# Kernel optimization log

Measured on AMD Instinct MI355X. Metric: run time of the kernel, lower is better.

Reference implementation:

```python
import math
import jax, jax.numpy as jnp
import numpy as np

B, S, D_MODEL = 4, 1024, 512
D_BAR, C_ONSET, N_HEADS = 256, 32, 8
T_ONSET, POOL = 8192, 8


def setup_inputs() -> dict:
    key = jax.random.key(0)
    ks = jax.random.split(key, 16)
    p = lambda i, shape: jax.random.normal(ks[i], shape, dtype=jnp.float32) * 0.05
    return {
        "token_embs": jax.random.normal(ks[0], (B, S, D_MODEL), dtype=jnp.float32),
        "onset_1d": jax.random.uniform(ks[1], (B, T_ONSET, C_ONSET), dtype=jnp.float32),
        "bar_mask": jax.random.bernoulli(ks[2], 0.0625, (B, S)),  # ~1 bar / 16 tokens
        "Wih_note": p(3, (3 * D_BAR, D_MODEL)),
        "Whh_note": p(4, (3 * D_BAR, D_BAR)),
        "bih_note": p(5, (3 * D_BAR,)),
        "bhh_note": p(6, (3 * D_BAR,)),
        "Wih_bar": p(7, (3 * D_BAR, D_BAR)),
        "Whh_bar": p(8, (3 * D_BAR, D_BAR)),
        "bih_bar": p(9, (3 * D_BAR,)),
        "bhh_bar": p(10, (3 * D_BAR,)),
        "Wq": p(11, (D_BAR, D_BAR)),
        "bq": p(12, (D_BAR,)),
        "Wk": p(13, (D_BAR, C_ONSET)),
        "bk": p(14, (D_BAR,)),
        "pos_bias_scale": jnp.float32(2.5),
    }


def _gru_cell(x, h, Wih, Whh, bih, bhh):
    # torch nn.GRU cell, gate order (r, z, n)
    gi = x @ Wih.T + bih
    gh = h @ Whh.T + bhh
    ir, iz, inn = jnp.split(gi, 3, axis=-1)
    hr, hz, hn = jnp.split(gh, 3, axis=-1)
    r = jax.nn.sigmoid(ir + hr)
    z = jax.nn.sigmoid(iz + hz)
    n = jnp.tanh(inn + r * hn)
    return (1.0 - z) * n + z * h


def _sinusoidal_pe(T, C, dtype):
    half = C // 2
    pos = jnp.arange(T, dtype=dtype)
    div = jnp.exp(jnp.arange(half, dtype=dtype) * (-math.log(10000.0) / half))
    ang = pos[:, None] * div[None, :]  # [T, half]
    # interleave sin/cos -> [T, C] (C even)
    return jnp.stack([jnp.sin(ang), jnp.cos(ang)], axis=-1).reshape(T, C)


def _forward(token_embs, onset_1d, bar_mask, Wih_note, Whh_note, bih_note, bhh_note,
             Wih_bar, Whh_bar, bih_bar, bhh_bar, Wq, bq, Wk, bk, pos_bias_scale):
    Bc, Sc, _ = token_embs.shape
    d_bar = Whh_bar.shape[1]
    H = N_HEADS
    dh = d_bar // H
    dtype = token_embs.dtype

    # --- audio keys: avg_pool1d(k=8,s=8) + sinusoidal PE + projection ---
    T = onset_1d.shape[1]
    pooled = onset_1d.reshape(Bc, T // POOL, POOL, onset_1d.shape[2]).mean(axis=2)  # [B,T_oct,C]
    T_oct = pooled.shape[1]
    pe = _sinusoidal_pe(T_oct, pooled.shape[2], dtype)
    K = (pooled + pe[None]) @ Wk.T + bk  # [B,T_oct,d_bar]

    # --- fused note-GRU / bar-GRU scan over sequence positions ---
    # Segment semantics: bar tokens are excluded from note-GRU segments; at a
    # <bar> position the note hidden (= bar summary; zero for empty segments)
    # feeds one bar-GRU step, then the note hidden resets to zero.
    def step(carry, xs):
        h_note, g_bar = carry
        x, m = xs  # x: [B,D], m: [B] bool
        h_next = _gru_cell(x, h_note, Wih_note, Whh_note, bih_note, bhh_note)
        g_next = _gru_cell(h_note, g_bar, Wih_bar, Whh_bar, bih_bar, bhh_bar)
        m_ = m[:, None]
        g_out = jnp.where(m_, g_next, g_bar)
        h_out = jnp.where(m_, jnp.zeros_like(h_next), h_next)
        return (h_out, g_out), g_out

    zeros = jnp.zeros((Bc, d_bar), dtype=dtype)
    (_, g_end), g_seq = jax.lax.scan(
        step, (zeros, zeros),
        (token_embs.transpose(1, 0, 2), bar_mask.T))
    h_bar_carried = g_seq.transpose(1, 0, 2)  # [B,S,d_bar]: h_bar after most recent bar <= s
    h_bar_final = g_end[None]                 # [1,B,d_bar]

    # --- cross-attention com_t (computed densely, masked to <bar> positions) ---
    Q = (h_bar_carried @ Wq.T + bq).reshape(Bc, Sc, H, dh)
    K4 = K.reshape(Bc, T_oct, H, dh)
    scores = jnp.einsum('bshd,bthd->bsht', Q, K4) / math.sqrt(dh)
    time_pos = jnp.linspace(0.0, 1.0, T_oct, dtype=dtype)
    scores = scores - pos_bias_scale * time_pos  # broadcast pos bias over t
    attn = jax.nn.softmax(scores, axis=-1)
    com = jnp.sum(attn.mean(axis=2) * time_pos, axis=-1)  # [B,S]
    com_t_all = jnp.where(bar_mask, com, 0.0)[..., None]  # [B,S,1]

    return com_t_all, h_bar_final, h_bar_carried


def reference(token_embs, onset_1d, bar_mask, Wih_note, Whh_note, bih_note, bhh_note,
              Wih_bar, Whh_bar, bih_bar, bhh_bar, Wq, bq, Wk, bk, pos_bias_scale):
    return _forward(token_embs, onset_1d, bar_mask, Wih_note, Whh_note, bih_note, bhh_note,
                    Wih_bar, Whh_bar, bih_bar, bhh_bar, Wq, bq, Wk, bk, pos_bias_scale)
```

## Files before the change

### kernel.cpp

```cpp
#include <hip/hip_runtime.h>
#include <hip/hip_bf16.h>
#include <math.h>

#define NB 4
#define SEQ 1024
#define DM 512
#define DB 256
#define G3 768
#define CO 32
#define TONS 8192
#define POOLN 8
#define TOCT 1024
#define NH 8
#define DHD 32

#define RKT 5
#define LKT 3

#define OFF_GI     0u
#define OFF_GIBAR  3145728u
#define OFF_HEND   6291456u
#define OFF_GALL   7340032u
#define OFF_KMAT   8388608u
#define OFF_WFN    9437184u
#define OFF_WFB    9535488u
#define OFF_WFIHN  9633792u
#define OFF_WFIHB  9830400u
#define OFF_INT_BYTES 39714816u

#define OUT_FINAL 4096
#define OUT_CARR  5120

typedef __attribute__((ext_vector_type(8))) short short8v;
typedef __attribute__((ext_vector_type(4))) float f32x4;

__device__ __forceinline__ unsigned int bf16rne(float f) {
    unsigned int u = __float_as_uint(f);
    return (u + 0x7fffu + ((u >> 16) & 1u)) >> 16;
}
__device__ __forceinline__ float fsigm(float x) {
    return __fdividef(1.f, 1.f + __expf(-x));
}
__device__ __forceinline__ float ftanh(float x) {
    return 1.f - __fdividef(2.f, __expf(2.f * x) + 1.f);
}

__device__ void wfrag_job(const float* __restrict__ W, uint4* __restrict__ out,
                          int Kdim, int KTN, int idx) {
    if (idx >= 48 * KTN * 64) return;
    int lane = idx & 63;
    int TK = idx >> 6;
    int T = TK / KTN, Kt = TK % KTN;
    int row = 16 * T + (lane & 15);
    int kb = 32 * Kt + (lane >> 4) * 8;
    const float* wr = W + (size_t)row * Kdim + kb;
    uint4 u;
    u.x = bf16rne(wr[0]) | (bf16rne(wr[1]) << 16);
    u.y = bf16rne(wr[2]) | (bf16rne(wr[3]) << 16);
    u.z = bf16rne(wr[4]) | (bf16rne(wr[5]) << 16);
    u.w = bf16rne(wr[6]) | (bf16rne(wr[7]) << 16);
    out[idx] = u;
}

__global__ __launch_bounds__(256) void k_prep(const unsigned char* __restrict__ mraw,
        int* __restrict__ pos, int* __restrict__ lastk, int* __restrict__ nmask,
        int* __restrict__ sS, int* __restrict__ sLen, int* __restrict__ sC,
        int* __restrict__ nseg,
        const float* __restrict__ Whh_n, uint4* __restrict__ wfn,
        const float* __restrict__ Whh_b, uint4* __restrict__ wfb,
        const float* __restrict__ Wih_n, uint4* __restrict__ wfihn,
        const float* __restrict__ Wih_b, uint4* __restrict__ wfihb,
        const float* __restrict__ onset, const float* __restrict__ Wk,
        const float* __restrict__ bk, float* __restrict__ Kmat) {
    int bid = blockIdx.x;
    int tid = threadIdx.x;
    if (bid == 0) {
        __shared__ int rnz[8];
        __shared__ int gt1;
        __shared__ int mode;
        __shared__ int snm[NB];
        if (tid < 8) rnz[tid] = 0;
        if (tid == 0) gt1 = 0;
        __syncthreads();
        for (int i = tid; i < NB * SEQ; i += 256) {
            unsigned char v = mraw[i];
            if (v) {
                rnz[i & 7] = 1;
                if (v > 1) gt1 = 1;
            }
        }
        __syncthreads();
        if (tid == 0) {
            bool lowhalf = rnz[0] | rnz[1] | rnz[4] | rnz[5];
            bool hihalf  = rnz[2] | rnz[3] | rnz[6] | rnz[7];
            int m;
            if (hihalf && !lowhalf) {
                m = (rnz[2] | rnz[3]) ? 3 : 4;
            } else if (gt1) {
                m = 5;
            } else if (rnz[1] | rnz[3] | rnz[5] | rnz[7]) {
                m = 0;
            } else if (rnz[4]) {
                m = 1;
            } else if (rnz[0]) {
                m = 2;
            } else {
                m = 0;
            }
            mode = m;
        }
        __syncthreads();
        if (tid < NB) {
            int b = tid;
            int cnt = 0;
            for (int t = 0; t < SEQ; ++t) {
                int idx = b * SEQ + t;
                int mv;
                switch (mode) {
                    case 0:  mv = mraw[idx] != 0; break;
                    case 1:  mv = ((const int*)mraw)[idx] != 0; break;
                    case 2:  mv = ((const long long*)mraw)[idx] != 0LL; break;
                    case 3:  mv = ((const float*)mraw)[idx] != 0.f; break;
                    case 4:  mv = ((const double*)mraw)[idx] != 0.0; break;
                    default: mv = ((const unsigned short*)mraw)[idx] != 0; break;
                }
                if (mv) { pos[b * SEQ + cnt] = t; ++cnt; }
                lastk[idx] = cnt - 1;
            }
            nmask[b] = cnt;
            snm[b] = cnt;
        }
        __syncthreads();
        if (tid < NB) {
            int b = tid;
            int base = 0;
            for (int x = 0; x < b; ++x) base += snm[x];
            int cnt = snm[b];
            for (int k = 0; k < cnt; ++k) {
                int e = pos[b * SEQ + k];
                int s = (k == 0) ? 0 : (pos[b * SEQ + k - 1] + 1);
                sS[base + k]   = b * SEQ + s;
                sLen[base + k] = e - s;
                sC[base + k]   = b * SEQ + k;
            }
        }
        __syncthreads();
        if (tid == 0) {
            int t = 0;
            for (int x = 0; x < NB; ++x) t += snm[x];
            *nseg = t;
        }
    } else if (bid <= 96) {
        wfrag_job(Whh_n, wfn, DB, 8, (bid - 1) * 256 + tid);
    } else if (bid <= 192) {
        wfrag_job(Whh_b, wfb, DB, 8, (bid - 97) * 256 + tid);
    } else if (bid <= 384) {
        wfrag_job(Wih_n, wfihn, DM, 16, (bid - 193) * 256 + tid);
    } else if (bid <= 480) {
        wfrag_job(Wih_b, wfihb, DB, 8, (bid - 385) * 256 + tid);
    } else {
        __shared__ float xin[4][CO];
        int sub = tid >> 6;
        int t64 = tid & 63;
        int bt = (bid - 481) * 4 + sub;
        int b = bt >> 10, t = bt & 1023;
        if (t64 < CO) {
            float s = 0.f;
            const float* base = onset + ((size_t)b * TONS + (size_t)t * POOLN) * CO + t64;
#pragma unroll
            for (int p = 0; p < POOLN; ++p) s += base[p * CO];
            s *= (1.f / POOLN);
            int j = t64 >> 1;
            float dv = __expf(-logf(10000.f) * (float)j / 16.f);
            float ang = (float)t * dv;
            s += (t64 & 1) ? __cosf(ang) : __sinf(ang);
            xin[sub][t64] = s;
        }
        __syncthreads();
        for (int n = t64; n < DB; n += 64) {
            float acc = bk[n];
            const float* wr = Wk + (size_t)n * CO;
#pragma unroll
            for (int c = 0; c < CO; ++c) acc += xin[sub][c] * wr[c];
            Kmat[(size_t)bt * DB + n] = acc;
        }
    }
}

template<bool LIM>
__global__ __launch_bounds__(256) void k_gemm_mfma(int Kdim, int KTN,
        const float* __restrict__ A, const uint4* __restrict__ Bf,
        const float* __restrict__ bias, float* __restrict__ C,
        const int* __restrict__ nmask) {
    int bm = blockIdx.x * 64, bn = blockIdx.y * 64;
    if (LIM) {
        int b = bm >> 10;
        if ((bm & 1023) >= nmask[b]) return;
    }
    int tid = threadIdx.x;
    int w = tid >> 6;
    int lane = tid & 63;
    int arow = bm + 16 * w + (lane & 15);
    int kofs = (lane >> 4) * 8;
    f32x4 acc[4];
#pragma unroll
    for (int nt = 0; nt < 4; ++nt) acc[nt] = (f32x4){0.f, 0.f, 0.f, 0.f};
    for (int kc = 0; kc < KTN; ++kc) {
        const float* ap = A + (size_t)arow * Kdim + kc * 32 + kofs;
        float4 p0 = *reinterpret_cast<const float4*>(ap);
        float4 p1 = *reinterpret_cast<const float4*>(ap + 4);
        uint4 au;
        au.x = bf16rne(p0.x) | (bf16rne(p0.y) << 16);
        au.y = bf16rne(p0.z) | (bf16rne(p0.w) << 16);
        au.z = bf16rne(p1.x) | (bf16rne(p1.y) << 16);
        au.w = bf16rne(p1.z) | (bf16rne(p1.w) << 16);
        short8v a = __builtin_bit_cast(short8v, au);
#pragma unroll
        for (int nt = 0; nt < 4; ++nt) {
            int T = (bn >> 4) + nt;
            uint4 u = Bf[(size_t)(T * KTN + kc) * 64 + lane];
            short8v bv = __builtin_bit_cast(short8v, u);
            acc[nt] = __builtin_amdgcn_mfma_f32_16x16x32_bf16(a, bv, acc[nt], 0, 0, 0);
        }
    }
    int crow = bm + 16 * w + (lane >> 4) * 4;
#pragma unroll
    for (int nt = 0; nt < 4; ++nt) {
        int col = bn + 16 * nt + (lane & 15);
        float bv = bias[col];
#pragma unroll
        for (int r = 0; r < 4; ++r)
            C[(size_t)(crow + r) * G3 + col] = acc[nt][r] + bv;
    }
}

template<int MODE>
__global__ __launch_bounds__(512, 1) void k_gru(
        const uint4* __restrict__ wf, const float* __restrict__ bhh,
        const float* __restrict__ gx_src,
        const int* __restrict__ sS, const int* __restrict__ sLen,
        const int* __restrict__ sC, const int* __restrict__ nseg_p,
        const int* __restrict__ nmask, float* __restrict__ outp) {
    int bg = blockIdx.x;
    int nseg = (MODE == 0) ? *nseg_p : NB;
    if (16 * bg >= nseg) return;
    int tid = threadIdx.x;
    int w = tid >> 6;
    int lane = tid & 63;
    int lhi = lane >> 4, c = lane & 15;

    __shared__ __align__(16) unsigned short hfrag[8 * 64 * 8];
    __shared__ __align__(16) uint4 wlds[8 * 6 * LKT * 64];

    uint4 wreg[6][RKT];
#pragma unroll
    for (int t = 0; t < 6; ++t) {
        int T = 16 * (t >> 1) + 2 * w + (t & 1);
#pragma unroll
        for (int kt = 0; kt < RKT; ++kt)
            wreg[t][kt] = wf[(size_t)(T * 8 + kt) * 64 + lane];
#pragma unroll
        for (int kt = 0; kt < LKT; ++kt)
            wlds[((w * 6 + t) * LKT + kt) * 64 + lane] = wf[(size_t)(T * 8 + RKT + kt) * 64 + lane];
    }

    int ss_r[4], len_r[4], sc_r[4];
#pragma unroll
    for (int r = 0; r < 4; ++r) {
        int m = 4 * lhi + r;
        int gs = 16 * bg + m;
        if (MODE == 0) {
            bool v = gs < nseg;
            ss_r[r]  = v ? sS[gs] : 0;
            len_r[r] = v ? sLen[gs] : 0;
            sc_r[r]  = v ? sC[gs] : 0;
        } else {
            bool v = m < NB;
            ss_r[r]  = v ? m * SEQ : 0;
            len_r[r] = v ? nmask[m] : 0;
            sc_r[r]  = 0;
        }
    }
    int mx = 0;
    for (int q = 0; q < 16; ++q) {
        int gs = 16 * bg + q;
        int L = (MODE == 0) ? ((gs < nseg) ? sLen[gs] : 0)
                            : ((q < NB) ? nmask[q] : 0);
        mx = max(mx, L);
    }
    float bh[3][2];
#pragma unroll
    for (int g = 0; g < 3; ++g)
#pragma unroll
        for (int ii = 0; ii < 2; ++ii)
            bh[g][ii] = bhh[g * 256 + 32 * w + 16 * ii + c];
    float h[4][2] = {};

#define LOADGX(dst, step)                                                        \
    {                                                                            \
        int i_ = (step);                                                         \
        _Pragma("unroll")                                                        \
        for (int r = 0; r < 4; ++r) {                                            \
            int row = (i_ < len_r[r]) ? (ss_r[r] + i_) : ss_r[r];                \
            const float* gp = gx_src + (size_t)row * G3 + 32 * w + c;            \
            _Pragma("unroll")                                                    \
            for (int g = 0; g < 3; ++g)                                          \
                _Pragma("unroll")                                                \
                for (int ii = 0; ii < 2; ++ii)                                   \
                    dst[g][ii][r] = gp[g * 256 + 16 * ii];                       \
        }                                                                        \
    }

#define GRU_STEP(I, GX)                                                          \
    {                                                                            \
        int i_ = (I);                                                            \
        f32x4 acc[6];                                                            \
        _Pragma("unroll")                                                        \
        for (int t = 0; t < 6; ++t) acc[t] = (f32x4){0.f, 0.f, 0.f, 0.f};        \
        if (i_ > 0) {                                                            \
            const short8v* hf8 = (const short8v*)hfrag;                          \
            _Pragma("unroll")                                                    \
            for (int kt = 0; kt < 8; ++kt) {                                     \
                short8v a = hf8[kt * 64 + lane];                                 \
                if (kt < RKT) {                                                  \
                    _Pragma("unroll")                                            \
                    for (int t = 0; t < 6; ++t) {                                \
                        short8v bv = __builtin_bit_cast(short8v, wreg[t][kt]);   \
                        acc[t] = __builtin_amdgcn_mfma_f32_16x16x32_bf16(        \
                                a, bv, acc[t], 0, 0, 0);                         \
                    }                                                            \
                } else {                                                         \
                    _Pragma("unroll")                                            \
                    for (int t = 0; t < 6; ++t) {                                \
                        uint4 u = wlds[((w * 6 + t) * LKT + (kt - RKT)) * 64 + lane]; \
                        short8v bv = __builtin_bit_cast(short8v, u);             \
                        acc[t] = __builtin_amdgcn_mfma_f32_16x16x32_bf16(        \
                                a, bv, acc[t], 0, 0, 0);                         \
                    }                                                            \
                }                                                                \
            }                                                                    \
        }                                                                        \
        _Pragma("unroll")                                                        \
        for (int r = 0; r < 4; ++r) {                                            \
            _Pragma("unroll")                                                    \
            for (int ii = 0; ii < 2; ++ii) {                                     \
                float rr = fsigm(GX[0][ii][r] + bh[0][ii] + acc[0 + ii][r]);     \
                float zz = fsigm(GX[1][ii][r] + bh[1][ii] + acc[2 + ii][r]);     \
                float nn = ftanh(GX[2][ii][r] + rr * (bh[2][ii] + acc[4 + ii][r])); \
                float hv = (1.f - zz) * nn + zz * h[r][ii];                      \
                bool act = i_ < len_r[r];                                        \
                hv = act ? hv : h[r][ii];                                        \
                h[r][ii] = hv;                                                   \
                if (MODE == 1) {                                                 \
                    if (lhi == 0 && act) {                                       \
                        int j = 32 * w + 16 * ii + c;                            \
                        outp[(size_t)(ss_r[r] + i_) * DB + j] = hv;              \
                    }                                                            \
                }                                                                \
            }                                                                    \
        }                                                                        \
        __syncthreads();                                                         \
        _Pragma("unroll")                                                        \
        for (int r = 0; r < 4; ++r)                                              \
            _Pragma("unroll")                                                    \
            for (int ii = 0; ii < 2; ++ii) {                                     \
                int j = 32 * w + 16 * ii + c;                                    \
                int m = 4 * lhi + r;                                             \
                int lp = m + 16 * ((j >> 3) & 3);                                \
                hfrag[(size_t)(w * 64 + lp) * 8 + (j & 7)] =                     \
                    (unsigned short)bf16rne(h[r][ii]);                           \
            }                                                                    \
        __syncthreads();                                                         \
    }

    float gxa[3][2][4], gxb[3][2][4];
    LOADGX(gxa, 0)
    for (int i = 0; i < mx; i += 2) {
        LOADGX(gxb, i + 1)
        GRU_STEP(i, gxa)
        LOADGX(gxa, i + 2)
        GRU_STEP(i + 1, gxb)
    }
#undef LOADGX
#undef GRU_STEP
    if (MODE == 0) {
#pragma unroll
        for (int r = 0; r < 4; ++r) {
            int gs = 16 * bg + 4 * lhi + r;
            if (gs < nseg) {
#pragma unroll
                for (int ii = 0; ii < 2; ++ii)
                    outp[(size_t)sc_r[r] * DB + 32 * w + 16 * ii + c] = h[r][ii];
            }
        }
    }
}

__global__ __launch_bounds__(256) void k_fillattn(const float* __restrict__ gall,
        const int* __restrict__ lastk, const int* __restrict__ nmask,
        const int* __restrict__ pos,
        const float* __restrict__ Wq, const float* __restrict__ bq,
        const float* __restrict__ Kmat, const float* __restrict__ pbs_ptr,
        float* __restrict__ out) {
    int bt = blockIdx.x;
    int b = bt >> 10, t = bt & 1023;
    int tid = threadIdx.x;
    int lk = lastk[bt];
    float v = (lk >= 0) ? gall[((size_t)b * SEQ + lk) * DB + tid] : 0.f;
    out[OUT_CARR + (size_t)bt * DB + tid] = v;
    if (tid == 0) out[bt] = 0.f;
    if (t == 0) {
        int nm = nmask[b];
        float fv = (nm > 0) ? gall[((size_t)b * SEQ + nm - 1) * DB + tid] : 0.f;
        out[OUT_FINAL + b * DB + tid] = fv;
    }
    bool is_mask = (lk >= 0) && (pos[b * SEQ + lk] == t);
    if (!is_mask) return;
    int k = lk;
    __shared__ float q[DB];
    __shared__ float grow[DB];
    __shared__ float sc[NH][TOCT];
    __shared__ float comh[NH];
    grow[tid] = gall[((size_t)b * SEQ + k) * DB + tid];
    __syncthreads();
    {
        float acc = bq[tid];
        const float* wr = Wq + (size_t)tid * DB;
#pragma unroll 4
        for (int j = 0; j < DB; ++j) acc += grow[j] * wr[j];
        q[tid] = acc;
    }
    __syncthreads();
    float pbs = *pbs_ptr;
    const float scale = 0.17677669529663687f;
    for (int tt = tid; tt < TOCT; tt += 256) {
        const float* kr = Kmat + ((size_t)b * TOCT + tt) * DB;
        float tp = (float)tt * (1.f / 1023.f);
#pragma unroll
        for (int h = 0; h < NH; ++h) {
            float acc = 0.f;
#pragma unroll
            for (int d = 0; d < DHD; ++d) acc += q[h * DHD + d] * kr[h * DHD + d];
            sc[h][tt] = acc * scale - pbs * tp;
        }
    }
    __syncthreads();
    int hh = tid >> 5, l = tid & 31;
    float mx = -1e30f;
    for (int tt = l; tt < TOCT; tt += 32) mx = fmaxf(mx, sc[hh][tt]);
#pragma unroll
    for (int o = 16; o > 0; o >>= 1) mx = fmaxf(mx, __shfl_xor(mx, o, 32));
    float se = 0.f, sw = 0.f;
    for (int tt = l; tt < TOCT; tt += 32) {
        float e = __expf(sc[hh][tt] - mx);
        se += e;
        sw += e * ((float)tt * (1.f / 1023.f));
    }
#pragma unroll
    for (int o = 16; o > 0; o >>= 1) { se += __shfl_xor(se, o, 32); sw += __shfl_xor(sw, o, 32); }
    if (l == 0) comh[hh] = sw / se;
    __syncthreads();
    if (tid == 0) {
        float cm = 0.f;
#pragma unroll
        for (int h = 0; h < NH; ++h) cm += comh[h];
        out[b * SEQ + t] = cm * (1.f / NH);
    }
}

extern "C" void kernel_launch(void* const* d_in, const int* in_sizes, int n_in,
                              void* d_out, int out_size, void* d_ws, size_t ws_size,
                              hipStream_t stream) {
    const float* te    = (const float*)d_in[0];
    const float* onset = (const float*)d_in[1];
    const unsigned char* mask = (const unsigned char*)d_in[2];
    const float* Wih_n = (const float*)d_in[3];
    const float* Whh_n = (const float*)d_in[4];
    const float* bih_n = (const float*)d_in[5];
    const float* bhh_n = (const float*)d_in[6];
    const float* Wih_b = (const float*)d_in[7];
    const float* Whh_b = (const float*)d_in[8];
    const float* bih_b = (const float*)d_in[9];
    const float* bhh_b = (const float*)d_in[10];
    const float* Wq    = (const float*)d_in[11];
    const float* bq    = (const float*)d_in[12];
    const float* Wk    = (const float*)d_in[13];
    const float* bk    = (const float*)d_in[14];
    const float* pbs   = (const float*)d_in[15];
    float* out = (float*)d_out;

    float* ws    = (float*)d_ws;
    float* gi    = ws + OFF_GI;
    float* gibar = ws + OFF_GIBAR;
    float* hend  = ws + OFF_HEND;
    float* gall  = ws + OFF_GALL;
    float* kmat  = ws + OFF_KMAT;
    uint4* wfn   = (uint4*)(ws + OFF_WFN);
    uint4* wfb   = (uint4*)(ws + OFF_WFB);
    uint4* wfihn = (uint4*)(ws + OFF_WFIHN);
    uint4* wfihb = (uint4*)(ws + OFF_WFIHB);
    int* ipos    = (int*)((char*)d_ws + OFF_INT_BYTES);
    int* ilastk  = ipos + NB * SEQ;
    int* inmask  = ilastk + NB * SEQ;
    int* isS     = inmask + NB;
    int* isLen   = isS + NB * SEQ;
    int* isC     = isLen + NB * SEQ;
    int* inseg   = isC + NB * SEQ;

    k_prep<<<1505, 256, 0, stream>>>(mask, ipos, ilastk, inmask, isS, isLen, isC, inseg,
                                     Whh_n, wfn, Whh_b, wfb, Wih_n, wfihn, Wih_b, wfihb,
                                     onset, Wk, bk, kmat);
    k_gemm_mfma<false><<<dim3(64, 12), 256, 0, stream>>>(DM, 16, te, wfihn, bih_n, gi, inmask);
    k_gru<0><<<256, 512, 0, stream>>>(wfn, bhh_n, gi, isS, isLen, isC, inseg, inmask, hend);
    k_gemm_mfma<true><<<dim3(64, 12), 256, 0, stream>>>(DB, 8, hend, wfihb, bih_b, gibar, inmask);
    k_gru<1><<<1, 512, 0, stream>>>(wfb, bhh_b, gibar, isS, isLen, isC, inseg, inmask, gall);
    k_fillattn<<<NB * SEQ, 256, 0, stream>>>(gall, ilastk, inmask, ipos, Wq, bq, kmat, pbs, out);
}
```

Measured before the change: 964.8 us.

## Fuse note GRU, bar input projection and bar GRU with flag-based streaming

Merges the note-level GRU, the bar input-projection GEMM and the bar-level GRU into a single persistent launch. Block 0 runs the bar GRU and polls per-segment ready flags, while the other blocks run note segments, compute the bar gate inputs in-register with MFMA, and publish them with release stores. This lets the serial bar recurrence overlap with note-GRU work and removes two launches and the intermediate h_end buffer. The cost is inter-block spin-waiting, which depends on all blocks being co-resident and risks a deadlock or a guarded timeout. Block 0 is also the bar GRU, and it contends for the device with 256 note blocks.

```diff
diff --git a/kernel.cpp b/kernel.cpp
--- a/kernel.cpp
+++ b/kernel.cpp
@@ -65,7 +65,7 @@
 __global__ __launch_bounds__(256) void k_prep(const unsigned char* __restrict__ mraw,
         int* __restrict__ pos, int* __restrict__ lastk, int* __restrict__ nmask,
         int* __restrict__ sS, int* __restrict__ sLen, int* __restrict__ sC,
-        int* __restrict__ nseg,
+        int* __restrict__ nseg, int* __restrict__ ibase, int* __restrict__ iflag,
         const float* __restrict__ Whh_n, uint4* __restrict__ wfn,
         const float* __restrict__ Whh_b, uint4* __restrict__ wfb,
         const float* __restrict__ Wih_n, uint4* __restrict__ wfihn,
@@ -75,6 +75,7 @@
     int bid = blockIdx.x;
     int tid = threadIdx.x;
     if (bid == 0) {
+        for (int i = tid; i < NB * SEQ; i += 256) iflag[i] = 0;
         __shared__ int rnz[8];
         __shared__ int gt1;
         __shared__ int mode;
@@ -135,6 +136,7 @@
             int b = tid;
             int base = 0;
             for (int x = 0; x < b; ++x) base += snm[x];
+            ibase[b] = base;
             int cnt = snm[b];
             for (int k = 0; k < cnt; ++k) {
                 int e = pos[b * SEQ + k];
@@ -187,16 +189,10 @@
     }
 }
 
-template<bool LIM>
 __global__ __launch_bounds__(256) void k_gemm_mfma(int Kdim, int KTN,
         const float* __restrict__ A, const uint4* __restrict__ Bf,
-        const float* __restrict__ bias, float* __restrict__ C,
-        const int* __restrict__ nmask) {
+        const float* __restrict__ bias, float* __restrict__ C) {
     int bm = blockIdx.x * 64, bn = blockIdx.y * 64;
-    if (LIM) {
-        int b = bm >> 10;
-        if ((bm & 1023) >= nmask[b]) return;
-    }
     int tid = threadIdx.x;
     int w = tid >> 6;
     int lane = tid & 63;
@@ -234,16 +230,17 @@
     }
 }
 
-template<int MODE>
-__global__ __launch_bounds__(512, 1) void k_gru(
-        const uint4* __restrict__ wf, const float* __restrict__ bhh,
-        const float* __restrict__ gx_src,
+__global__ __launch_bounds__(512, 1) void k_gru_fused(
+        const uint4* __restrict__ wfn, const float* __restrict__ bhh_n,
+        const float* __restrict__ gi,
+        const uint4* __restrict__ wfb, const float* __restrict__ bhh_b,
+        float* __restrict__ gibar,
+        const uint4* __restrict__ wfihb, const float* __restrict__ bih_b,
         const int* __restrict__ sS, const int* __restrict__ sLen,
         const int* __restrict__ sC, const int* __restrict__ nseg_p,
-        const int* __restrict__ nmask, float* __restrict__ outp) {
-    int bg = blockIdx.x;
-    int nseg = (MODE == 0) ? *nseg_p : NB;
-    if (16 * bg >= nseg) return;
+        const int* __restrict__ nmask, const int* __restrict__ ibase,
+        int* __restrict__ iflag, float* __restrict__ gall) {
+    int bid = blockIdx.x;
     int tid = threadIdx.x;
     int w = tid >> 6;
     int lane = tid & 63;
@@ -252,6 +249,15 @@
     __shared__ __align__(16) unsigned short hfrag[8 * 64 * 8];
     __shared__ __align__(16) uint4 wlds[8 * 6 * LKT * 64];
 
+    const int MODE = (bid == 0) ? 1 : 0;
+    int bg = bid - 1;
+    int nseg = *nseg_p;
+    if (MODE == 0 && 16 * bg >= nseg) return;
+
+    const uint4* wf = (MODE == 0) ? wfn : wfb;
+    const float* bhh = (MODE == 0) ? bhh_n : bhh_b;
+    const float* gx_src = (MODE == 0) ? gi : gibar;
+
     uint4 wreg[6][RKT];
 #pragma unroll
     for (int t = 0; t < 6; ++t) {
@@ -268,8 +274,8 @@
 #pragma unroll
     for (int r = 0; r < 4; ++r) {
         int m = 4 * lhi + r;
-        int gs = 16 * bg + m;
         if (MODE == 0) {
+            int gs = 16 * bg + m;
             bool v = gs < nseg;
             ss_r[r]  = v ? sS[gs] : 0;
             len_r[r] = v ? sLen[gs] : 0;
@@ -283,9 +289,13 @@
     }
     int mx = 0;
     for (int q = 0; q < 16; ++q) {
-        int gs = 16 * bg + q;
-        int L = (MODE == 0) ? ((gs < nseg) ? sLen[gs] : 0)
-                            : ((q < NB) ? nmask[q] : 0);
+        int L;
+        if (MODE == 0) {
+            int gs = 16 * bg + q;
+            L = (gs < nseg) ? sLen[gs] : 0;
+        } else {
+            L = (q < NB) ? nmask[q] : 0;
+        }
         mx = max(mx, L);
     }
     float bh[3][2];
@@ -295,6 +305,24 @@
         for (int ii = 0; ii < 2; ++ii)
             bh[g][ii] = bhh[g * 256 + 32 * w + 16 * ii + c];
     float h[4][2] = {};
+
+#define POLLSTEP(X)                                                              \
+    if (MODE == 1) {                                                             \
+        if (tid < NB) {                                                          \
+            int nm = nmask[tid];                                                 \
+            if (nm > 0) {                                                        \
+                int x_ = (X); if (x_ > nm - 1) x_ = nm - 1;                      \
+                int idx = ibase[tid] + x_;                                       \
+                long long guard = 0;                                             \
+                while (__hip_atomic_load(&iflag[idx], __ATOMIC_ACQUIRE,          \
+                                         __HIP_MEMORY_SCOPE_AGENT) == 0) {       \
+                    if (++guard > 200000000LL) break;                            \
+                    __builtin_amdgcn_s_sleep(2);                                 \
+                }                                                                \
+            }                                                                    \
+        }                                                                        \
+        __syncthreads();                                                         \
+    }
 
 #define LOADGX(dst, step)                                                        \
     {                                                                            \
@@ -354,7 +382,7 @@
                 if (MODE == 1) {                                                 \
                     if (lhi == 0 && act) {                                       \
                         int j = 32 * w + 16 * ii + c;                            \
-                        outp[(size_t)(ss_r[r] + i_) * DB + j] = hv;              \
+                        gall[(size_t)(ss_r[r] + i_) * DB + j] = hv;              \
                     }                                                            \
                 }                                                                \
             }                                                                    \
@@ -374,24 +402,55 @@
     }
 
     float gxa[3][2][4], gxb[3][2][4];
+    POLLSTEP(0)
     LOADGX(gxa, 0)
     for (int i = 0; i < mx; i += 2) {
+        POLLSTEP(i + 1)
         LOADGX(gxb, i + 1)
         GRU_STEP(i, gxa)
+        POLLSTEP(i + 2)
         LOADGX(gxa, i + 2)
         GRU_STEP(i + 1, gxb)
     }
+#undef POLLSTEP
 #undef LOADGX
 #undef GRU_STEP
+
     if (MODE == 0) {
-#pragma unroll
-        for (int r = 0; r < 4; ++r) {
-            int gs = 16 * bg + 4 * lhi + r;
-            if (gs < nseg) {
-#pragma unroll
-                for (int ii = 0; ii < 2; ++ii)
-                    outp[(size_t)sc_r[r] * DB + 32 * w + 16 * ii + c] = h[r][ii];
+        f32x4 acc[6];
+#pragma unroll
+        for (int t = 0; t < 6; ++t) acc[t] = (f32x4){0.f, 0.f, 0.f, 0.f};
+        const short8v* hf8 = (const short8v*)hfrag;
+#pragma unroll
+        for (int kt = 0; kt < 8; ++kt) {
+            short8v a = hf8[kt * 64 + lane];
+#pragma unroll
+            for (int t = 0; t < 6; ++t) {
+                int T = 16 * (t >> 1) + 2 * w + (t & 1);
+                uint4 u = wfihb[(size_t)(T * 8 + kt) * 64 + lane];
+                short8v bv = __builtin_bit_cast(short8v, u);
+                acc[t] = __builtin_amdgcn_mfma_f32_16x16x32_bf16(a, bv, acc[t], 0, 0, 0);
             }
+        }
+#pragma unroll
+        for (int t = 0; t < 6; ++t) {
+            int T = 16 * (t >> 1) + 2 * w + (t & 1);
+            int col = 16 * T + c;
+            float bv = bih_b[col];
+#pragma unroll
+            for (int r = 0; r < 4; ++r) {
+                int gs = 16 * bg + 4 * lhi + r;
+                if (gs < nseg)
+                    gibar[(size_t)sc_r[r] * G3 + col] = acc[t][r] + bv;
+            }
+        }
+        __syncthreads();
+        __threadfence();
+        if (tid < 16) {
+            int gs = 16 * bg + tid;
+            if (gs < nseg)
+                __hip_atomic_store(&iflag[gs], 1, __ATOMIC_RELEASE,
+                                   __HIP_MEMORY_SCOPE_AGENT);
         }
     }
 }
@@ -492,7 +551,6 @@
     float* ws    = (float*)d_ws;
     float* gi    = ws + OFF_GI;
     float* gibar = ws + OFF_GIBAR;
-    float* hend  = ws + OFF_HEND;
     float* gall  = ws + OFF_GALL;
     float* kmat  = ws + OFF_KMAT;
     uint4* wfn   = (uint4*)(ws + OFF_WFN);
@@ -506,13 +564,17 @@
     int* isLen   = isS + NB * SEQ;
     int* isC     = isLen + NB * SEQ;
     int* inseg   = isC + NB * SEQ;
+    int* ibase   = inseg + 1;
+    int* iflag   = ibase + 8;
 
     k_prep<<<1505, 256, 0, stream>>>(mask, ipos, ilastk, inmask, isS, isLen, isC, inseg,
+                                     ibase, iflag,
                                      Whh_n, wfn, Whh_b, wfb, Wih_n, wfihn, Wih_b, wfihb,
                                      onset, Wk, bk, kmat);
-    k_gemm_mfma<false><<<dim3(64, 12), 256, 0, stream>>>(DM, 16, te, wfihn, bih_n, gi, inmask);
-    k_gru<0><<<256, 512, 0, stream>>>(wfn, bhh_n, gi, isS, isLen, isC, inseg, inmask, hend);
-    k_gemm_mfma<true><<<dim3(64, 12), 256, 0, stream>>>(DB, 8, hend, wfihb, bih_b, gibar, inmask);
-    k_gru<1><<<1, 512, 0, stream>>>(wfb, bhh_b, gibar, isS, isLen, isC, inseg, inmask, gall);
+    k_gemm_mfma<<<dim3(64, 12), 256, 0, stream>>>(DM, 16, te, wfihn, bih_n, gi);
+    k_gru_fused<<<257, 512, 0, stream>>>(wfn, bhh_n, gi, wfb, bhh_b, gibar,
+                                         wfihb, bih_b,
+                                         isS, isLen, isC, inseg, inmask, ibase,
+                                         iflag, gall);
     k_fillattn<<<NB * SEQ, 256, 0, stream>>>(gall, ilastk, inmask, ipos, Wq, bq, kmat, pbs, out);
 }
```

Result: slower. 994.1 us (+3.0%).
